# Performance work log

Measured on AMD Instinct MI355X. Metric: run time of the kernel, lower is better.

Reference implementation:

```python
import jax, jax.numpy as jnp
import numpy as np
import math

B, S, NUM_HEADS, HEAD_SIZE = 4, 2048, 16, 64
EMB = NUM_HEADS * HEAD_SIZE  # 1024


def setup_inputs() -> dict:
    key = jax.random.key(0)
    k0, k1, k2, k3 = jax.random.split(key, 4)
    scale = 1.0 / math.sqrt(EMB)
    return {
        "hidden_states": jax.random.normal(k0, (B, S, EMB), dtype=jnp.float32),
        "qkv_w": jax.random.normal(k1, (EMB, 3 * EMB), dtype=jnp.float32) * scale,
        "qkv_b": jnp.zeros((3 * EMB,), dtype=jnp.float32),
        "wo_w": jax.random.normal(k2, (EMB, EMB), dtype=jnp.float32) * scale,
        "wo_b": jnp.zeros((EMB,), dtype=jnp.float32),
        "mask": jax.random.randint(k3, (B, S), 0, 2, dtype=jnp.int64)
        if jax.config.jax_enable_x64 else jax.random.randint(k3, (B, S), 0, 2, dtype=jnp.int32),
    }


def reference(hidden_states, qkv_w, qkv_b, wo_w, wo_b, mask):
    b, s, e = hidden_states.shape
    h, d = NUM_HEADS, HEAD_SIZE
    qkv = hidden_states @ qkv_w + qkv_b            # [b, s, 3e]
    q, k, v = jnp.split(qkv, 3, axis=-1)
    # split heads: [b, s, e] -> [b, h, s, d]
    split = lambda t: t.reshape(b, s, h, d).transpose(0, 2, 1, 3)
    q, k, v = split(q), split(k), split(v)
    # naive attention: full [b, h, s, s] score matrix, scaled by sqrt(head_size)
    scores = jnp.einsum("bhqd,bhkd->bhqk", q, k) / jnp.sqrt(jnp.asarray(d, q.dtype))
    # torch code repeats the [b, s] padding mask into [b, h, s, s]; it masks KEYS:
    # position j with mask[b, j] == 0 is -inf for all queries and heads.
    scores = jnp.where(mask[:, None, None, :] == 0, -jnp.inf, scores)
    attn = jax.nn.softmax(scores, axis=-1)
    out = jnp.einsum("bhqk,bhkd->bhqd", attn, v)   # [b, h, s, d]
    out = out.transpose(0, 2, 1, 3).reshape(b, s, e)  # merge heads
    return out @ wo_w + wo_b
```

## Files before the change

kernel.cpp:

```cpp
#include <hip/hip_runtime.h>
#include <math.h>

typedef __bf16 bf16;
typedef __bf16 bf16x4 __attribute__((ext_vector_type(4)));
typedef __bf16 bf16x8 __attribute__((ext_vector_type(8)));
typedef _Float16 f16;
typedef _Float16 f16x4 __attribute__((ext_vector_type(4)));
typedef _Float16 f16x8 __attribute__((ext_vector_type(8)));
typedef float floatx4 __attribute__((ext_vector_type(4)));
typedef float floatx16 __attribute__((ext_vector_type(16)));
typedef short shortx4 __attribute__((ext_vector_type(4)));

#define MFMA_BF16(a, b, c) __builtin_amdgcn_mfma_f32_16x16x32_bf16((a), (b), (c), 0, 0, 0)
#define MFMA_F16(a, b, c) __builtin_amdgcn_mfma_f32_16x16x32_f16((a), (b), (c), 0, 0, 0)
#define MFMA32_BF16(a, b, c) __builtin_amdgcn_mfma_f32_32x32x16_bf16((a), (b), (c), 0, 0, 0)

__device__ inline floatx16 MFMA_PV32(bf16x4 a, bf16x4 b, floatx16 c) {
#if __has_builtin(__builtin_amdgcn_mfma_f32_32x32x8_bf16)
  return __builtin_amdgcn_mfma_f32_32x32x8_bf16(a, b, c, 0, 0, 0);
#elif __has_builtin(__builtin_amdgcn_mfma_f32_32x32x8bf16_1k)
  shortx4 as, bs;
  __builtin_memcpy(&as, &a, 8);
  __builtin_memcpy(&bs, &b, 8);
  return __builtin_amdgcn_mfma_f32_32x32x8bf16_1k(as, bs, c, 0, 0, 0);
#else
  bf16 z = (bf16)0.f;
  bf16x8 a8 = {a[0], a[1], a[2], a[3], z, z, z, z};
  bf16x8 b8 = {b[0], b[1], b[2], b[3], z, z, z, z};
  return MFMA32_BF16(a8, b8, c);
#endif
}

__device__ inline void gload16(const void* g, void* l) {
  __builtin_amdgcn_global_load_lds(
      (const __attribute__((address_space(1))) void*)g,
      (__attribute__((address_space(3))) void*)l, 16, 0, 0);
}

__device__ inline int detect_i64(const void* m_) {
  const unsigned int* m = (const unsigned int*)m_;
  unsigned int o = 0;
  for (int i = 1; i < 256; i += 2) o |= m[i];
  return o == 0;
}

__device__ inline int xcd_swizzle(int bid, int nwg) {
  return (bid & 7) * (nwg >> 3) + (bid >> 3);
}

__global__ void wsplit(const float* __restrict__ in, f16* __restrict__ out,
                       int R, int C) {
  __shared__ float tile[32][33];
  int bx = blockIdx.x * 32, by = blockIdx.y * 32;
  int tx = threadIdx.x, ty = threadIdx.y;
#pragma unroll
  for (int i = 0; i < 32; i += 8)
    tile[ty + i][tx] = in[(size_t)(by + ty + i) * C + bx + tx];
  __syncthreads();
#pragma unroll
  for (int i = 0; i < 32; i += 8) {
    float x = tile[tx][ty + i];
    size_t oi = (size_t)(bx + ty + i) * R + by + tx;
    out[oi] = (f16)x;
  }
}

template <int MODE>
__global__ __launch_bounds__(256) void gemm(
    const void* __restrict__ Av, const f16* __restrict__ Bg,
    const float* __restrict__ bias, void* __restrict__ Cq,
    bf16* __restrict__ Ck, bf16* __restrict__ Cv, int M, int N, int K) {
  constexpr int APAD = (MODE == 1) ? 40 : 32;
  __shared__ __align__(16) f16 Ah[2][128][APAD];
  __shared__ __align__(16) f16 Bs[2][128][32];

  int tid = threadIdx.x;
  int wave = tid >> 6, lane = tid & 63;
  int quad = lane >> 4, c = lane & 15;
  int wrow = (wave >> 1) * 64, wcol = (wave & 1) * 64;

  int nwg = gridDim.x * gridDim.y;
  int bid = blockIdx.x + gridDim.x * blockIdx.y;
  int nb = xcd_swizzle(bid, nwg);
  int m0 = (nb / gridDim.x) * 128, n0 = (nb % gridDim.x) * 128;

  int srow = lane >> 2;
  int ql8 = (((lane & 3) ^ ((lane >> 3) & 3)) * 8);
  int rswz = (c >> 1) & 3;

  floatx4 zero4 = {0.f, 0.f, 0.f, 0.f};
  floatx4 acc[4][4];
#pragma unroll
  for (int i = 0; i < 4; ++i)
#pragma unroll
    for (int j = 0; j < 4; ++j) acc[i][j] = zero4;

  floatx4 aR[4];

#define STAGE_B(buf, kk)                                                    \
  {                                                                         \
    _Pragma("unroll") for (int u = 0; u < 2; ++u) {                         \
      int ch = wave * 2 + u;                                                \
      size_t gi = (size_t)(n0 + ch * 16 + srow) * K + (kk) + ql8;           \
      gload16(&Bg[gi], &Bs[buf][ch * 16][0]);                               \
    }                                                                       \
  }
#define STAGE_A_DMA(buf, kk)                                                \
  {                                                                         \
    _Pragma("unroll") for (int u = 0; u < 2; ++u) {                         \
      int ch = wave * 2 + u;                                                \
      size_t gi = (size_t)(m0 + ch * 16 + srow) * K + (kk) + ql8;           \
      gload16((const f16*)Av + gi, &Ah[buf][ch * 16][0]);                   \
    }                                                                       \
  }
#define ISSUE_A(kk)                                                         \
  {                                                                         \
    const float* Af = (const float*)Av;                                     \
    _Pragma("unroll") for (int p = 0; p < 2; ++p) {                         \
      int off = p * 2048 + tid * 8;                                         \
      int r = off >> 5, cc = off & 31;                                      \
      size_t gi = (size_t)(m0 + r) * K + (kk) + cc;                         \
      aR[p * 2] = *(const floatx4*)&Af[gi];                                 \
      aR[p * 2 + 1] = *(const floatx4*)&Af[gi + 4];                         \
    }                                                                       \
  }
#define WRITE_A(buf)                                                        \
  {                                                                         \
    _Pragma("unroll") for (int p = 0; p < 2; ++p) {                         \
      int off = p * 2048 + tid * 8;                                         \
      int r = off >> 5, cc = off & 31;                                      \
      f16x8 h;                                                              \
      _Pragma("unroll") for (int uu = 0; uu < 4; ++uu) {                    \
        h[uu] = (f16)aR[p * 2][uu];                                         \
        h[4 + uu] = (f16)aR[p * 2 + 1][uu];                                 \
      }                                                                     \
      *(f16x8*)&Ah[buf][r][cc] = h;                                         \
    }                                                                       \
  }

  STAGE_B(0, 0);
  if constexpr (MODE == 1) {
    ISSUE_A(0);
    WRITE_A(0);
  } else {
    STAGE_A_DMA(0, 0);
  }
  __syncthreads();

  int nk = K / 32;
  int cur = 0;
  for (int t = 0; t < nk; ++t) {
    int kn = (t + 1) * 32;
    bool has_next = (t + 1 < nk);
    if (has_next) {
      STAGE_B(cur ^ 1, kn);
      if constexpr (MODE == 1) {
        ISSUE_A(kn);
      } else {
        STAGE_A_DMA(cur ^ 1, kn);
      }
    }

    f16x8 ah[4], bh[4];
#pragma unroll
    for (int i = 0; i < 4; ++i) {
      if constexpr (MODE == 1)
        ah[i] = *(const f16x8*)&Ah[cur][wrow + i * 16 + c][quad * 8];
      else
        ah[i] = *(const f16x8*)&Ah[cur][wrow + i * 16 + c][(quad ^ rswz) * 8];
    }
#pragma unroll
    for (int j = 0; j < 4; ++j)
      bh[j] = *(const f16x8*)&Bs[cur][wcol + j * 16 + c][(quad ^ rswz) * 8];
#pragma unroll
    for (int i = 0; i < 4; ++i)
#pragma unroll
      for (int j = 0; j < 4; ++j)
        acc[i][j] = MFMA_F16(ah[i], bh[j], acc[i][j]);

    if (has_next) {
      if constexpr (MODE == 1) WRITE_A(cur ^ 1);
      __syncthreads();
      cur ^= 1;
    }
  }
#undef STAGE_B
#undef STAGE_A_DMA
#undef ISSUE_A
#undef WRITE_A

#pragma unroll
  for (int i = 0; i < 4; ++i) {
#pragma unroll
    for (int j = 0; j < 4; ++j) {
      int col = n0 + wcol + j * 16 + c;
      float bvv = bias[col];
#pragma unroll
      for (int r = 0; r < 4; ++r) {
        int row = m0 + wrow + i * 16 + quad * 4 + r;
        float v = acc[i][j][r] + bvv;
        if constexpr (MODE == 0) {
          ((float*)Cq)[(size_t)row * N + col] = v;
        } else {
          int which = col >> 10;
          int h = (col >> 6) & 15;
          int d = col & 63;
          int b = row >> 11;
          int s = row & 2047;
          if (which == 0) {
            ((bf16*)Cq)[((size_t)(b * 2048 + s)) * 1024 + h * 64 + d] = (bf16)v;
          } else if (which == 1) {
            Ck[((size_t)(b * 16 + h) * 2048 + s) * 64 + d] = (bf16)v;
          } else {
            Cv[((size_t)(b * 16 + h) * 64 + d) * 2048 + s] = (bf16)v;
          }
        }
      }
    }
  }
}

__global__ __launch_bounds__(256) void attn_fused(
    bf16* QO, const bf16* __restrict__ Kg, const bf16* __restrict__ Vg,
    const void* __restrict__ mask) {
  __shared__ __align__(16) bf16 Ks[64][72];
  __shared__ __align__(16) bf16 Vts[64][72];
  __shared__ __align__(16) float abuf_all[2048];

  const int i64 = detect_i64(mask);

  int tid = threadIdx.x;
  int wave = tid >> 6, lane = tid & 63;
  int l31 = lane & 31, hi = lane >> 5;

  int nwg = gridDim.x * gridDim.y;
  int bid = blockIdx.x + gridDim.x * blockIdx.y;
  int nb = xcd_swizzle(bid, nwg);
  int qt = nb & 15, bh = nb >> 4;

  int b = bh >> 4, h = bh & 15;
  int q0 = qt * 128;
  bf16* Qp = QO + (size_t)b * 2048 * 1024 + h * 64;
  const bf16* Kp = Kg + (size_t)bh * 2048 * 64;
  const bf16* Vp = Vg + (size_t)bh * 64 * 2048;

#pragma unroll
  for (int i = 0; i < 8; ++i) {
    int key = tid * 8 + i;
    int idx = b * 2048 + key;
    int mv = i64 ? (int)((const long long*)mask)[idx]
                 : ((const int*)mask)[idx];
    abuf_all[key] = mv ? -12.0f : -1e30f;
  }

  int qrow = q0 + wave * 32 + l31;
  bf16x8 qf[4];
#pragma unroll
  for (int ds = 0; ds < 4; ++ds)
    qf[ds] = *(const bf16x8*)&Qp[(size_t)qrow * 1024 + ds * 16 + hi * 8];

  floatx16 o[2];
#pragma unroll
  for (int dt = 0; dt < 2; ++dt)
#pragma unroll
    for (int i = 0; i < 16; ++i) o[dt][i] = 0.f;
  float lacc = 0.f;

#pragma unroll
  for (int p = 0; p < 2; ++p) {
    int off = p * 2048 + tid * 8;
    int r = off >> 6, cc = off & 63;
    *(bf16x8*)&Ks[r][cc] = *(const bf16x8*)&Kp[(size_t)r * 64 + cc];
  }
  __syncthreads();

  bf16x4 pk[8];

  for (int kt = 0; kt < 32; ++kt) {
    int k0 = kt * 64;

    bf16x8 vstage[2];
#pragma unroll
    for (int p = 0; p < 2; ++p) {
      int off = p * 2048 + tid * 8;
      int r = off >> 6, cc = off & 63;
      vstage[p] = *(const bf16x8*)&Vp[(size_t)r * 2048 + k0 + cc];
    }

#pragma unroll
    for (int t2 = 0; t2 < 2; ++t2) {
      floatx16 sr;
#pragma unroll
      for (int i = 0; i < 16; ++i) sr[i] = 0.f;
#pragma unroll
      for (int ds = 0; ds < 4; ++ds) {
        bf16x8 ak = *(const bf16x8*)&Ks[t2 * 32 + l31][ds * 16 + hi * 8];
        sr = MFMA32_BF16(ak, qf[ds], sr);
      }
#pragma unroll
      for (int s = 0; s < 4; ++s) {
        floatx4 am = *(const floatx4*)&abuf_all[k0 + t2 * 32 + s * 8 + hi * 4];
        bf16x4 p4;
#pragma unroll
        for (int j = 0; j < 4; ++j) {
          float pv = __expf(fmaf(sr[s * 4 + j], 0.125f, am[j]));
          lacc += pv;
          p4[j] = (bf16)pv;
        }
        pk[t2 * 4 + s] = p4;
      }
    }

#pragma unroll
    for (int p = 0; p < 2; ++p) {
      int off = p * 2048 + tid * 8;
      int r = off >> 6, cc = off & 63;
      *(bf16x8*)&Vts[r][cc] = vstage[p];
    }
    __syncthreads();

    bf16x8 kstage[2];
    bool more = (kt + 1) < 32;
    int kn = k0 + 64;
    if (more) {
#pragma unroll
      for (int p = 0; p < 2; ++p) {
        int off = p * 2048 + tid * 8;
        int r = off >> 6, cc = off & 63;
        kstage[p] = *(const bf16x8*)&Kp[(size_t)(kn + r) * 64 + cc];
      }
    }

#pragma unroll
    for (int ss = 0; ss < 8; ++ss) {
#pragma unroll
      for (int dt = 0; dt < 2; ++dt) {
        bf16x4 av = *(const bf16x4*)&Vts[dt * 32 + l31][ss * 8 + hi * 4];
        o[dt] = MFMA_PV32(av, pk[ss], o[dt]);
      }
    }

    if (more) {
#pragma unroll
      for (int p = 0; p < 2; ++p) {
        int off = p * 2048 + tid * 8;
        int r = off >> 6, cc = off & 63;
        *(bf16x8*)&Ks[r][cc] = kstage[p];
      }
      __syncthreads();
    }
  }

  lacc += __shfl_xor(lacc, 32, 64);
  float inv = 1.0f / fmaxf(lacc, 1e-30f);

#pragma unroll
  for (int dt = 0; dt < 2; ++dt) {
#pragma unroll
    for (int t = 0; t < 4; ++t) {
      f16x4 out;
#pragma unroll
      for (int j = 0; j < 4; ++j) out[j] = (f16)(o[dt][t * 4 + j] * inv);
      int d0 = dt * 32 + t * 8 + hi * 4;
      *(f16x4*)((f16*)&Qp[(size_t)qrow * 1024] + d0) = out;
    }
  }
}

extern "C" void kernel_launch(void* const* d_in, const int* in_sizes, int n_in,
                              void* d_out, int out_size, void* d_ws, size_t ws_size,
                              hipStream_t stream) {
  (void)in_sizes; (void)n_in; (void)out_size;
  const float* hs    = (const float*)d_in[0];
  const float* qkv_w = (const float*)d_in[1];
  const float* qkv_b = (const float*)d_in[2];
  const float* wo_w  = (const float*)d_in[3];
  const float* wo_b  = (const float*)d_in[4];
  const void*  mask  = d_in[5];

  if (ws_size < 33554432) return;

  bf16* kbuf = (bf16*)d_ws;
  f16*  wq   = (f16*)((char*)d_ws + 16777216);
  f16*  wo   = (f16*)((char*)d_ws + 16777216 + 6291456);
  bf16* vbuf = (bf16*)d_out + (size_t)8388608;
  f16*  obuf = (f16*)d_ws;

  wsplit<<<dim3(96, 32), dim3(32, 8), 0, stream>>>(qkv_w, wq, 1024, 3072);
  wsplit<<<dim3(32, 32), dim3(32, 8), 0, stream>>>(wo_w, wo, 1024, 1024);

  gemm<1><<<dim3(24, 64), 256, 0, stream>>>(
      hs, wq, qkv_b, d_out, kbuf, vbuf, 8192, 3072, 1024);

  attn_fused<<<dim3(16, 64), 256, 0, stream>>>(
      (bf16*)d_out, kbuf, vbuf, mask);

  (void)hipMemcpyAsync(d_ws, d_out, (size_t)16777216, hipMemcpyDeviceToDevice,
                       stream);

  gemm<0><<<dim3(8, 64), 256, 0, stream>>>(
      obuf, wo, wo_b, d_out, nullptr, nullptr, 8192, 1024, 1024);
}
```

Measured before the change: 362.9 us.

## Double-buffer K/V tiles via async global-to-LDS loads with XOR swizzle

Replaces register-staged K/V copies into padded LDS with direct global_load_lds into double-buffered, XOR-swizzled LDS tiles. The next tile's load is issued before the current tile's compute, so there is one barrier per iteration instead of two. The exponent also switches from __expf to a native exp2 with a log2(e)-folded scale and mask offset. This uses more LDS and relies on the swizzle staying bank-conflict free, and the barrier placement must keep the buffers race-free.

```diff
diff --git a/kernel.cpp b/kernel.cpp
--- a/kernel.cpp
+++ b/kernel.cpp
@@ -28,6 +28,14 @@
   bf16x8 a8 = {a[0], a[1], a[2], a[3], z, z, z, z};
   bf16x8 b8 = {b[0], b[1], b[2], b[3], z, z, z, z};
   return MFMA32_BF16(a8, b8, c);
+#endif
+}
+
+__device__ inline float fast_exp2(float x) {
+#if __has_builtin(__builtin_amdgcn_exp2f)
+  return __builtin_amdgcn_exp2f(x);
+#else
+  return exp2f(x);
 #endif
 }
 
@@ -223,8 +231,8 @@
 __global__ __launch_bounds__(256) void attn_fused(
     bf16* QO, const bf16* __restrict__ Kg, const bf16* __restrict__ Vg,
     const void* __restrict__ mask) {
-  __shared__ __align__(16) bf16 Ks[64][72];
-  __shared__ __align__(16) bf16 Vts[64][72];
+  __shared__ __align__(16) bf16 KsL[2][4096];
+  __shared__ __align__(16) bf16 VtsL[2][4096];
   __shared__ __align__(16) float abuf_all[2048];
 
   const int i64 = detect_i64(mask);
@@ -232,6 +240,7 @@
   int tid = threadIdx.x;
   int wave = tid >> 6, lane = tid & 63;
   int l31 = lane & 31, hi = lane >> 5;
+  int lx = l31 & 7;
 
   int nwg = gridDim.x * gridDim.y;
   int bid = blockIdx.x + gridDim.x * blockIdx.y;
@@ -244,13 +253,27 @@
   const bf16* Kp = Kg + (size_t)bh * 2048 * 64;
   const bf16* Vp = Vg + (size_t)bh * 64 * 2048;
 
+  int ri = lane >> 3;
+  int si = lane & 7;
+  int scol = (si ^ ri) * 8;
+
+#define STAGE_KV(buf, kk)                                                   \
+  {                                                                         \
+    _Pragma("unroll") for (int u = 0; u < 2; ++u) {                         \
+      int ch = wave * 2 + u;                                                \
+      int row = ch * 8 + ri;                                                \
+      gload16(&Kp[(size_t)((kk) + row) * 64 + scol], &KsL[buf][ch * 512]);  \
+      gload16(&Vp[(size_t)row * 2048 + (kk) + scol], &VtsL[buf][ch * 512]); \
+    }                                                                       \
+  }
+
 #pragma unroll
   for (int i = 0; i < 8; ++i) {
     int key = tid * 8 + i;
     int idx = b * 2048 + key;
     int mv = i64 ? (int)((const long long*)mask)[idx]
                  : ((const int*)mask)[idx];
-    abuf_all[key] = mv ? -12.0f : -1e30f;
+    abuf_all[key] = mv ? -17.3123404907f : -1e30f;
   }
 
   int qrow = q0 + wave * 32 + l31;
@@ -266,26 +289,17 @@
     for (int i = 0; i < 16; ++i) o[dt][i] = 0.f;
   float lacc = 0.f;
 
-#pragma unroll
-  for (int p = 0; p < 2; ++p) {
-    int off = p * 2048 + tid * 8;
-    int r = off >> 6, cc = off & 63;
-    *(bf16x8*)&Ks[r][cc] = *(const bf16x8*)&Kp[(size_t)r * 64 + cc];
-  }
+  STAGE_KV(0, 0);
   __syncthreads();
 
   bf16x4 pk[8];
+  int cur = 0;
 
   for (int kt = 0; kt < 32; ++kt) {
     int k0 = kt * 64;
-
-    bf16x8 vstage[2];
-#pragma unroll
-    for (int p = 0; p < 2; ++p) {
-      int off = p * 2048 + tid * 8;
-      int r = off >> 6, cc = off & 63;
-      vstage[p] = *(const bf16x8*)&Vp[(size_t)r * 2048 + k0 + cc];
-    }
+    bool more = (kt + 1) < 32;
+
+    if (more) STAGE_KV(cur ^ 1, k0 + 64);
 
 #pragma unroll
     for (int t2 = 0; t2 < 2; ++t2) {
@@ -294,7 +308,8 @@
       for (int i = 0; i < 16; ++i) sr[i] = 0.f;
 #pragma unroll
       for (int ds = 0; ds < 4; ++ds) {
-        bf16x8 ak = *(const bf16x8*)&Ks[t2 * 32 + l31][ds * 16 + hi * 8];
+        bf16x8 ak = *(const bf16x8*)&KsL[cur][(t2 * 32 + l31) * 64 +
+                                             (((ds * 2 + hi) ^ lx) * 8)];
         sr = MFMA32_BF16(ak, qf[ds], sr);
       }
 #pragma unroll
@@ -303,7 +318,7 @@
         bf16x4 p4;
 #pragma unroll
         for (int j = 0; j < 4; ++j) {
-          float pv = __expf(fmaf(sr[s * 4 + j], 0.125f, am[j]));
+          float pv = fast_exp2(fmaf(sr[s * 4 + j], 0.1803368801f, am[j]));
           lacc += pv;
           p4[j] = (bf16)pv;
         }
@@ -312,44 +327,21 @@
     }
 
 #pragma unroll
-    for (int p = 0; p < 2; ++p) {
-      int off = p * 2048 + tid * 8;
-      int r = off >> 6, cc = off & 63;
-      *(bf16x8*)&Vts[r][cc] = vstage[p];
-    }
-    __syncthreads();
-
-    bf16x8 kstage[2];
-    bool more = (kt + 1) < 32;
-    int kn = k0 + 64;
+    for (int ss = 0; ss < 8; ++ss) {
+#pragma unroll
+      for (int dt = 0; dt < 2; ++dt) {
+        bf16x4 av = *(const bf16x4*)&VtsL[cur][(dt * 32 + l31) * 64 +
+                                              ((ss ^ lx) * 8) + hi * 4];
+        o[dt] = MFMA_PV32(av, pk[ss], o[dt]);
+      }
+    }
+
     if (more) {
-#pragma unroll
-      for (int p = 0; p < 2; ++p) {
-        int off = p * 2048 + tid * 8;
-        int r = off >> 6, cc = off & 63;
-        kstage[p] = *(const bf16x8*)&Kp[(size_t)(kn + r) * 64 + cc];
-      }
-    }
-
-#pragma unroll
-    for (int ss = 0; ss < 8; ++ss) {
-#pragma unroll
-      for (int dt = 0; dt < 2; ++dt) {
-        bf16x4 av = *(const bf16x4*)&Vts[dt * 32 + l31][ss * 8 + hi * 4];
-        o[dt] = MFMA_PV32(av, pk[ss], o[dt]);
-      }
-    }
-
-    if (more) {
-#pragma unroll
-      for (int p = 0; p < 2; ++p) {
-        int off = p * 2048 + tid * 8;
-        int r = off >> 6, cc = off & 63;
-        *(bf16x8*)&Ks[r][cc] = kstage[p];
-      }
       __syncthreads();
-    }
-  }
+      cur ^= 1;
+    }
+  }
+#undef STAGE_KV
 
   lacc += __shfl_xor(lacc, 32, 64);
   float inv = 1.0f / fmaxf(lacc, 1e-30f);
```

New measurement: 366.1 us. About the same (+0.9%).

## Pre-convert hidden states to fp16 in halves and DMA-load A in QKV GEMM; use exp2

Applied to the files above, without the earlier changes.

Adds a separate conversion kernel that turns hidden_states into fp16, working on half the batch at a time in a workspace region, so the QKV GEMM can stage A with direct global-to-LDS loads in the same way it stages B, instead of loading fp32 through registers and converting there. The GEMM is launched twice, once per half, with a row offset. The attention softmax swaps __expf for a hardware exp2 with rescaled constants. The cost is an extra pass over the fp32 input and extra launches, which may offset the gain from the simpler GEMM pipeline.

```diff
diff --git a/kernel.cpp b/kernel.cpp
--- a/kernel.cpp
+++ b/kernel.cpp
@@ -31,6 +31,14 @@
 #endif
 }
 
+__device__ inline float fast_exp2(float x) {
+#if __has_builtin(__builtin_amdgcn_exp2f)
+  return __builtin_amdgcn_exp2f(x);
+#else
+  return exp2f(x);
+#endif
+}
+
 __device__ inline void gload16(const void* g, void* l) {
   __builtin_amdgcn_global_load_lds(
       (const __attribute__((address_space(1))) void*)g,
@@ -65,13 +73,26 @@
   }
 }
 
+__global__ __launch_bounds__(256) void hconv(const float* __restrict__ in,
+                                             f16* __restrict__ out) {
+  int idx = (blockIdx.x * 256 + threadIdx.x) * 16;
+#pragma unroll
+  for (int u = 0; u < 4; ++u) {
+    floatx4 v = *(const floatx4*)&in[idx + u * 4];
+    f16x4 h;
+#pragma unroll
+    for (int j = 0; j < 4; ++j) h[j] = (f16)v[j];
+    *(f16x4*)&out[idx + u * 4] = h;
+  }
+}
+
 template <int MODE>
 __global__ __launch_bounds__(256) void gemm(
-    const void* __restrict__ Av, const f16* __restrict__ Bg,
+    const f16* __restrict__ Av, const f16* __restrict__ Bg,
     const float* __restrict__ bias, void* __restrict__ Cq,
-    bf16* __restrict__ Ck, bf16* __restrict__ Cv, int M, int N, int K) {
-  constexpr int APAD = (MODE == 1) ? 40 : 32;
-  __shared__ __align__(16) f16 Ah[2][128][APAD];
+    bf16* __restrict__ Ck, bf16* __restrict__ Cv, int M, int N, int K,
+    int row_base) {
+  __shared__ __align__(16) f16 Ah[2][128][32];
   __shared__ __align__(16) f16 Bs[2][128][32];
 
   int tid = threadIdx.x;
@@ -95,80 +116,30 @@
 #pragma unroll
     for (int j = 0; j < 4; ++j) acc[i][j] = zero4;
 
-  floatx4 aR[4];
-
-#define STAGE_B(buf, kk)                                                    \
+#define STAGE_AB(buf, kk)                                                   \
   {                                                                         \
     _Pragma("unroll") for (int u = 0; u < 2; ++u) {                         \
       int ch = wave * 2 + u;                                                \
-      size_t gi = (size_t)(n0 + ch * 16 + srow) * K + (kk) + ql8;           \
-      gload16(&Bg[gi], &Bs[buf][ch * 16][0]);                               \
+      size_t gb = (size_t)(n0 + ch * 16 + srow) * K + (kk) + ql8;           \
+      gload16(&Bg[gb], &Bs[buf][ch * 16][0]);                               \
+      size_t ga = (size_t)(m0 + ch * 16 + srow) * K + (kk) + ql8;           \
+      gload16(&Av[ga], &Ah[buf][ch * 16][0]);                               \
     }                                                                       \
   }
-#define STAGE_A_DMA(buf, kk)                                                \
-  {                                                                         \
-    _Pragma("unroll") for (int u = 0; u < 2; ++u) {                         \
-      int ch = wave * 2 + u;                                                \
-      size_t gi = (size_t)(m0 + ch * 16 + srow) * K + (kk) + ql8;           \
-      gload16((const f16*)Av + gi, &Ah[buf][ch * 16][0]);                   \
-    }                                                                       \
-  }
-#define ISSUE_A(kk)                                                         \
-  {                                                                         \
-    const float* Af = (const float*)Av;                                     \
-    _Pragma("unroll") for (int p = 0; p < 2; ++p) {                         \
-      int off = p * 2048 + tid * 8;                                         \
-      int r = off >> 5, cc = off & 31;                                      \
-      size_t gi = (size_t)(m0 + r) * K + (kk) + cc;                         \
-      aR[p * 2] = *(const floatx4*)&Af[gi];                                 \
-      aR[p * 2 + 1] = *(const floatx4*)&Af[gi + 4];                         \
-    }                                                                       \
-  }
-#define WRITE_A(buf)                                                        \
-  {                                                                         \
-    _Pragma("unroll") for (int p = 0; p < 2; ++p) {                         \
-      int off = p * 2048 + tid * 8;                                         \
-      int r = off >> 5, cc = off & 31;                                      \
-      f16x8 h;                                                              \
-      _Pragma("unroll") for (int uu = 0; uu < 4; ++uu) {                    \
-        h[uu] = (f16)aR[p * 2][uu];                                         \
-        h[4 + uu] = (f16)aR[p * 2 + 1][uu];                                 \
-      }                                                                     \
-      *(f16x8*)&Ah[buf][r][cc] = h;                                         \
-    }                                                                       \
-  }
-
-  STAGE_B(0, 0);
-  if constexpr (MODE == 1) {
-    ISSUE_A(0);
-    WRITE_A(0);
-  } else {
-    STAGE_A_DMA(0, 0);
-  }
+
+  STAGE_AB(0, 0);
   __syncthreads();
 
   int nk = K / 32;
   int cur = 0;
   for (int t = 0; t < nk; ++t) {
-    int kn = (t + 1) * 32;
     bool has_next = (t + 1 < nk);
-    if (has_next) {
-      STAGE_B(cur ^ 1, kn);
-      if constexpr (MODE == 1) {
-        ISSUE_A(kn);
-      } else {
-        STAGE_A_DMA(cur ^ 1, kn);
-      }
-    }
+    if (has_next) STAGE_AB(cur ^ 1, (t + 1) * 32);
 
     f16x8 ah[4], bh[4];
 #pragma unroll
-    for (int i = 0; i < 4; ++i) {
-      if constexpr (MODE == 1)
-        ah[i] = *(const f16x8*)&Ah[cur][wrow + i * 16 + c][quad * 8];
-      else
-        ah[i] = *(const f16x8*)&Ah[cur][wrow + i * 16 + c][(quad ^ rswz) * 8];
-    }
+    for (int i = 0; i < 4; ++i)
+      ah[i] = *(const f16x8*)&Ah[cur][wrow + i * 16 + c][(quad ^ rswz) * 8];
 #pragma unroll
     for (int j = 0; j < 4; ++j)
       bh[j] = *(const f16x8*)&Bs[cur][wcol + j * 16 + c][(quad ^ rswz) * 8];
@@ -179,15 +150,11 @@
         acc[i][j] = MFMA_F16(ah[i], bh[j], acc[i][j]);
 
     if (has_next) {
-      if constexpr (MODE == 1) WRITE_A(cur ^ 1);
       __syncthreads();
       cur ^= 1;
     }
   }
-#undef STAGE_B
-#undef STAGE_A_DMA
-#undef ISSUE_A
-#undef WRITE_A
+#undef STAGE_AB
 
 #pragma unroll
   for (int i = 0; i < 4; ++i) {
@@ -197,7 +164,7 @@
       float bvv = bias[col];
 #pragma unroll
       for (int r = 0; r < 4; ++r) {
-        int row = m0 + wrow + i * 16 + quad * 4 + r;
+        int row = row_base + m0 + wrow + i * 16 + quad * 4 + r;
         float v = acc[i][j][r] + bvv;
         if constexpr (MODE == 0) {
           ((float*)Cq)[(size_t)row * N + col] = v;
@@ -250,7 +217,7 @@
     int idx = b * 2048 + key;
     int mv = i64 ? (int)((const long long*)mask)[idx]
                  : ((const int*)mask)[idx];
-    abuf_all[key] = mv ? -12.0f : -1e30f;
+    abuf_all[key] = mv ? -17.3123404907f : -1e30f;
   }
 
   int qrow = q0 + wave * 32 + l31;
@@ -303,7 +270,7 @@
         bf16x4 p4;
 #pragma unroll
         for (int j = 0; j < 4; ++j) {
-          float pv = __expf(fmaf(sr[s * 4 + j], 0.125f, am[j]));
+          float pv = fast_exp2(fmaf(sr[s * 4 + j], 0.1803368801f, am[j]));
           lacc += pv;
           p4[j] = (bf16)pv;
         }
@@ -383,14 +350,18 @@
   bf16* kbuf = (bf16*)d_ws;
   f16*  wq   = (f16*)((char*)d_ws + 16777216);
   f16*  wo   = (f16*)((char*)d_ws + 16777216 + 6291456);
+  f16*  hs16 = (f16*)((char*)d_ws + 25165824);
   bf16* vbuf = (bf16*)d_out + (size_t)8388608;
   f16*  obuf = (f16*)d_ws;
 
   wsplit<<<dim3(96, 32), dim3(32, 8), 0, stream>>>(qkv_w, wq, 1024, 3072);
   wsplit<<<dim3(32, 32), dim3(32, 8), 0, stream>>>(wo_w, wo, 1024, 1024);
 
-  gemm<1><<<dim3(24, 64), 256, 0, stream>>>(
-      hs, wq, qkv_b, d_out, kbuf, vbuf, 8192, 3072, 1024);
+  for (int half = 0; half < 2; ++half) {
+    hconv<<<dim3(1024), 256, 0, stream>>>(hs + (size_t)half * 4194304, hs16);
+    gemm<1><<<dim3(24, 32), 256, 0, stream>>>(
+        hs16, wq, qkv_b, d_out, kbuf, vbuf, 4096, 3072, 1024, half * 4096);
+  }
 
   attn_fused<<<dim3(16, 64), 256, 0, stream>>>(
       (bf16*)d_out, kbuf, vbuf, mask);
@@ -399,5 +370,5 @@
                        stream);
 
   gemm<0><<<dim3(8, 64), 256, 0, stream>>>(
-      obuf, wo, wo_b, d_out, nullptr, nullptr, 8192, 1024, 1024);
-}
+      obuf, wo, wo_b, d_out, nullptr, nullptr, 8192, 1024, 1024, 0);
+}
```

Result: slower. 391.9 us (+8.0%).
